# Performance work log

Measured on AMD Instinct MI355X. Metric: run time of the kernel, lower is better.

The kernel has to match this reference:

```python
import jax, jax.numpy as jnp
import numpy as np


def setup_inputs() -> dict:
    key = jax.random.key(0)
    k_z, k_w1, k_b1, k_w2, k_b2 = jax.random.split(key, 5)
    latent_dim = 16
    N = 2048
    z = jax.random.normal(k_z, (N, latent_dim), dtype=jnp.float32)
    # torch.nn.Linear default init: U(-1/sqrt(fan_in), 1/sqrt(fan_in))
    lim1 = 1.0 / np.sqrt(2 * latent_dim)
    W1 = jax.random.uniform(k_w1, (2 * latent_dim, latent_dim), minval=-lim1, maxval=lim1, dtype=jnp.float32)
    b1 = jax.random.uniform(k_b1, (latent_dim,), minval=-lim1, maxval=lim1, dtype=jnp.float32)
    lim2 = 1.0 / np.sqrt(latent_dim)
    W2 = jax.random.uniform(k_w2, (latent_dim, 1), minval=-lim2, maxval=lim2, dtype=jnp.float32)
    b2 = jax.random.uniform(k_b2, (1,), minval=-lim2, maxval=lim2, dtype=jnp.float32)
    return {"z": z, "W1": W1, "b1": b1, "W2": W2, "b2": b2}


def reference(z, W1, b1, W2, b2):
    # Pairwise concat is equivalent to splitting W1 into the halves acting on
    # z_i and z_j; we still materialize the [N, N, D] hidden like the original
    # math, but avoid the explicit [N, N, 2D] concat buffer.
    W1_i, W1_j = W1[: z.shape[1]], W1[z.shape[1] :]  # each [D, D_hidden]
    hi = z @ W1_i  # [N, Dh]
    hj = z @ W1_j  # [N, Dh]
    h = jax.nn.relu(hi[:, None, :] + hj[None, :, :] + b1)  # [N, N, Dh]
    logits = h @ W2 + b2  # [N, N, 1]
    return jax.nn.sigmoid(logits[..., 0])  # [N, N]
```

## Files before the change

kernel.cpp:

```cpp
#include <hip/hip_runtime.h>
#include <math.h>

#define D  16
#define JT 256
#define TI 32

__global__ __launch_bounds__(256) void MLPDecoder_68092411511098_kernel(
    const float* __restrict__ z, const float* __restrict__ W1,
    const float* __restrict__ b1, const float* __restrict__ W2,
    const float* __restrict__ b2, float* __restrict__ out, int N)
{
    __shared__ float sW1[2 * D * D];
    __shared__ float sZi[TI * D];
    __shared__ float sGi[TI * D];

    const int tid   = threadIdx.x;
    const int jbase = blockIdx.x * JT;
    const int ibase = blockIdx.y * TI;

    sW1[tid]       = W1[tid];
    sW1[tid + 256] = W1[tid + 256];
    if (tid < (TI * D) / 4) {
        ((float4*)sZi)[tid] = ((const float4*)(z + (size_t)ibase * D))[tid];
    }
    __syncthreads();

    float zr[D];
    {
        const float4* zrow = (const float4*)(z + (size_t)(jbase + tid) * D);
        float4 a = zrow[0], b = zrow[1], c = zrow[2], e = zrow[3];
        zr[0]=a.x;  zr[1]=a.y;  zr[2]=a.z;  zr[3]=a.w;
        zr[4]=b.x;  zr[5]=b.y;  zr[6]=b.z;  zr[7]=b.w;
        zr[8]=c.x;  zr[9]=c.y;  zr[10]=c.z; zr[11]=c.w;
        zr[12]=e.x; zr[13]=e.y; zr[14]=e.z; zr[15]=e.w;
    }
    float gj[D];
    #pragma unroll
    for (int k = 0; k < D; ++k) {
        float acc = b1[k];
        #pragma unroll
        for (int m = 0; m < D; ++m)
            acc = fmaf(zr[m], sW1[(D + m) * D + k], acc);
        gj[k] = acc;
    }

    #pragma unroll
    for (int v = tid; v < TI * D; v += 256) {
        const int ii = v >> 4, k = v & (D - 1);
        float acc = 0.0f;
        #pragma unroll
        for (int m = 0; m < D; ++m)
            acc = fmaf(sZi[ii * D + m], sW1[m * D + k], acc);
        sGi[v] = acc;
    }

    float w2r[D];
    #pragma unroll
    for (int k = 0; k < D; ++k) w2r[k] = W2[k];
    const float b2s = b2[0];
    __syncthreads();

    float* orow = out + (size_t)ibase * N + jbase + tid;
    for (int ii = 0; ii < TI; ++ii) {
        const float4* g4 = (const float4*)(sGi + ii * D);
        float4 g0 = g4[0], g1 = g4[1], g2 = g4[2], g3 = g4[3];
        float gi[D] = {g0.x,g0.y,g0.z,g0.w, g1.x,g1.y,g1.z,g1.w,
                       g2.x,g2.y,g2.z,g2.w, g3.x,g3.y,g3.z,g3.w};
        float acc = b2s;
        #pragma unroll
        for (int k = 0; k < D; ++k) {
            float t = gi[k] + gj[k];
            acc = fmaf(fmaxf(t, 0.0f), w2r[k], acc);
        }
        const float e = __expf(-acc);
        orow[(size_t)ii * N] = __builtin_amdgcn_rcpf(1.0f + e);
    }
}

extern "C" void kernel_launch(void* const* d_in, const int* in_sizes, int n_in,
                              void* d_out, int out_size, void* d_ws, size_t ws_size,
                              hipStream_t stream) {
    const float* z  = (const float*)d_in[0];
    const float* W1 = (const float*)d_in[1];
    const float* b1 = (const float*)d_in[2];
    const float* W2 = (const float*)d_in[3];
    const float* b2 = (const float*)d_in[4];
    float* out = (float*)d_out;

    const int N = in_sizes[0] / D;
    dim3 grid(N / JT, N / TI);
    MLPDecoder_68092411511098_kernel<<<grid, dim3(256), 0, stream>>>(
        z, W1, b1, W2, b2, out, N);
}
```

Measured before the change: 80.73 us.

## Precompute projections in fp16 prep kernel and use packed fdot2 inner loop

Adds a prep kernel that computes the z·W1 halves (with b1 folded into Hi) once per row and stores them as packed fp16 in the workspace. The main kernel then only loads these and does packed half add, relu and fdot2 accumulation into fp32, instead of recomputing the j-side projection in every block. TI drops from 32 to 8, giving four times as many blocks. The costs are fp16 rounding of the hidden activations, which may loosen accuracy, plus an extra kernel launch.

```diff
diff --git a/kernel.cpp b/kernel.cpp
--- a/kernel.cpp
+++ b/kernel.cpp
@@ -3,74 +3,90 @@
 
 #define D  16
 #define JT 256
-#define TI 32
+#define TI 8
+
+typedef _Float16 half2v __attribute__((ext_vector_type(2)));
+union H2U { half2v h; unsigned int u; };
+
+__global__ __launch_bounds__(256) void prep_kernel(
+    const float* __restrict__ z, const float* __restrict__ W1,
+    const float* __restrict__ b1, const float* __restrict__ W2,
+    half2v* __restrict__ Hi, half2v* __restrict__ Hj, half2v* __restrict__ w2p)
+{
+    __shared__ float sZ[16 * D];
+    __shared__ float sW[2 * D * D];
+    const int tid = threadIdx.x;
+    const int rowbase = blockIdx.x * 16;
+    if (tid < 64)       ((float4*)sZ)[tid]      = ((const float4*)(z + (size_t)rowbase * D))[tid];
+    else if (tid < 192) ((float4*)sW)[tid - 64] = ((const float4*)W1)[tid - 64];
+    __syncthreads();
+
+    const int r  = tid >> 4;
+    const int u  = tid & 15;
+    const int hf = u >> 3;
+    const int p  = u & 7;
+    const int k0 = 2 * p, k1 = k0 + 1;
+
+    float a0 = 0.f, a1 = 0.f;
+    #pragma unroll
+    for (int m = 0; m < D; ++m) {
+        const float zf = sZ[r * D + m];
+        const float* wrow = &sW[(hf * D + m) * D];
+        a0 = fmaf(zf, wrow[k0], a0);
+        a1 = fmaf(zf, wrow[k1], a1);
+    }
+    if (hf == 0) { a0 += b1[k0]; a1 += b1[k1]; }
+
+    H2U hv; hv.h.x = (_Float16)a0; hv.h.y = (_Float16)a1;
+    (hf ? Hj : Hi)[(size_t)(rowbase + r) * 8 + p] = hv.h;
+
+    if (blockIdx.x == 0 && tid < 8) {
+        H2U wv; wv.h.x = (_Float16)W2[2 * tid]; wv.h.y = (_Float16)W2[2 * tid + 1];
+        w2p[tid] = wv.h;
+    }
+}
 
 __global__ __launch_bounds__(256) void MLPDecoder_68092411511098_kernel(
-    const float* __restrict__ z, const float* __restrict__ W1,
-    const float* __restrict__ b1, const float* __restrict__ W2,
-    const float* __restrict__ b2, float* __restrict__ out, int N)
+    const half2v* __restrict__ Hi, const half2v* __restrict__ Hj,
+    const half2v* __restrict__ w2p, const float* __restrict__ b2,
+    float* __restrict__ out, int N)
 {
-    __shared__ float sW1[2 * D * D];
-    __shared__ float sZi[TI * D];
-    __shared__ float sGi[TI * D];
-
+    __shared__ half2v sHi[TI * 8];
     const int tid   = threadIdx.x;
     const int jbase = blockIdx.x * JT;
     const int ibase = blockIdx.y * TI;
 
-    sW1[tid]       = W1[tid];
-    sW1[tid + 256] = W1[tid + 256];
-    if (tid < (TI * D) / 4) {
-        ((float4*)sZi)[tid] = ((const float4*)(z + (size_t)ibase * D))[tid];
+    if (tid < TI * 8) sHi[tid] = Hi[(size_t)ibase * 8 + tid];
+
+    half2v vj[8];
+    {
+        const uint4* src = (const uint4*)(Hj + (size_t)(jbase + tid) * 8);
+        union { uint4 q; half2v h[4]; } c0, c1;
+        c0.q = src[0]; c1.q = src[1];
+        vj[0]=c0.h[0]; vj[1]=c0.h[1]; vj[2]=c0.h[2]; vj[3]=c0.h[3];
+        vj[4]=c1.h[0]; vj[5]=c1.h[1]; vj[6]=c1.h[2]; vj[7]=c1.h[3];
     }
-    __syncthreads();
-
-    float zr[D];
-    {
-        const float4* zrow = (const float4*)(z + (size_t)(jbase + tid) * D);
-        float4 a = zrow[0], b = zrow[1], c = zrow[2], e = zrow[3];
-        zr[0]=a.x;  zr[1]=a.y;  zr[2]=a.z;  zr[3]=a.w;
-        zr[4]=b.x;  zr[5]=b.y;  zr[6]=b.z;  zr[7]=b.w;
-        zr[8]=c.x;  zr[9]=c.y;  zr[10]=c.z; zr[11]=c.w;
-        zr[12]=e.x; zr[13]=e.y; zr[14]=e.z; zr[15]=e.w;
-    }
-    float gj[D];
+    half2v w2v[8];
     #pragma unroll
-    for (int k = 0; k < D; ++k) {
-        float acc = b1[k];
-        #pragma unroll
-        for (int m = 0; m < D; ++m)
-            acc = fmaf(zr[m], sW1[(D + m) * D + k], acc);
-        gj[k] = acc;
-    }
-
-    #pragma unroll
-    for (int v = tid; v < TI * D; v += 256) {
-        const int ii = v >> 4, k = v & (D - 1);
-        float acc = 0.0f;
-        #pragma unroll
-        for (int m = 0; m < D; ++m)
-            acc = fmaf(sZi[ii * D + m], sW1[m * D + k], acc);
-        sGi[v] = acc;
-    }
-
-    float w2r[D];
-    #pragma unroll
-    for (int k = 0; k < D; ++k) w2r[k] = W2[k];
+    for (int p = 0; p < 8; ++p) w2v[p] = w2p[p];
     const float b2s = b2[0];
+    const half2v zero = {(_Float16)0.f, (_Float16)0.f};
     __syncthreads();
 
     float* orow = out + (size_t)ibase * N + jbase + tid;
+    #pragma unroll 2
     for (int ii = 0; ii < TI; ++ii) {
-        const float4* g4 = (const float4*)(sGi + ii * D);
-        float4 g0 = g4[0], g1 = g4[1], g2 = g4[2], g3 = g4[3];
-        float gi[D] = {g0.x,g0.y,g0.z,g0.w, g1.x,g1.y,g1.z,g1.w,
-                       g2.x,g2.y,g2.z,g2.w, g3.x,g3.y,g3.z,g3.w};
+        const half2v* hrow = &sHi[ii * 8];
         float acc = b2s;
         #pragma unroll
-        for (int k = 0; k < D; ++k) {
-            float t = gi[k] + gj[k];
-            acc = fmaf(fmaxf(t, 0.0f), w2r[k], acc);
+        for (int p = 0; p < 8; ++p) {
+            half2v s = hrow[p] + vj[p];
+            half2v r = __builtin_elementwise_max(s, zero);
+#if __has_builtin(__builtin_amdgcn_fdot2)
+            acc = __builtin_amdgcn_fdot2(r, w2v[p], acc, false);
+#else
+            acc += (float)r.x * (float)w2v[p].x + (float)r.y * (float)w2v[p].y;
+#endif
         }
         const float e = __expf(-acc);
         orow[(size_t)ii * N] = __builtin_amdgcn_rcpf(1.0f + e);
@@ -88,7 +104,14 @@
     float* out = (float*)d_out;
 
     const int N = in_sizes[0] / D;
+
+    half2v* Hi  = (half2v*)d_ws;
+    half2v* Hj  = Hi + (size_t)N * 8;
+    half2v* w2p = Hj + (size_t)N * 8;
+
+    prep_kernel<<<dim3(N / 16), dim3(256), 0, stream>>>(z, W1, b1, W2, Hi, Hj, w2p);
+
     dim3 grid(N / JT, N / TI);
     MLPDecoder_68092411511098_kernel<<<grid, dim3(256), 0, stream>>>(
-        z, W1, b1, W2, b2, out, N);
+        Hi, Hj, w2p, b2, out, N);
 }
```

Result: faster. 73.36 us (-9.1%).

## Use packed fp16 add/relu with fdot2 for inner MLP and shrink i-tile

Applied to the files above, without the earlier changes.

The hidden activations gi and gj and the W2 weights are converted to packed half2. The inner loop uses packed fp16 add and max plus the fdot2 instruction with fp32 accumulation, which roughly halves the ALU instruction count per output. The i-tile drops from 32 to 16 rows, so the grid has more blocks, and launch bounds request 4 blocks per SM. The shared-memory prologue is reorganized so the z row load overlaps the staging of W1 and z_i, and b1 moves onto the gi side. The cost is reduced precision in the hidden layer, plus recomputing gj for twice as many blocks.

```diff
diff --git a/kernel.cpp b/kernel.cpp
--- a/kernel.cpp
+++ b/kernel.cpp
@@ -3,27 +3,22 @@
 
 #define D  16
 #define JT 256
-#define TI 32
+#define TI 16
 
-__global__ __launch_bounds__(256) void MLPDecoder_68092411511098_kernel(
+typedef _Float16 half2v __attribute__((ext_vector_type(2)));
+
+__global__ __launch_bounds__(256, 4) void MLPDecoder_68092411511098_kernel(
     const float* __restrict__ z, const float* __restrict__ W1,
     const float* __restrict__ b1, const float* __restrict__ W2,
     const float* __restrict__ b2, float* __restrict__ out, int N)
 {
-    __shared__ float sW1[2 * D * D];
-    __shared__ float sZi[TI * D];
-    __shared__ float sGi[TI * D];
+    __shared__ float  sW1[2 * D * D];
+    __shared__ float  sZi[TI * D];
+    __shared__ half2v sGi[TI * 8];
 
     const int tid   = threadIdx.x;
     const int jbase = blockIdx.x * JT;
     const int ibase = blockIdx.y * TI;
-
-    sW1[tid]       = W1[tid];
-    sW1[tid + 256] = W1[tid + 256];
-    if (tid < (TI * D) / 4) {
-        ((float4*)sZi)[tid] = ((const float4*)(z + (size_t)ibase * D))[tid];
-    }
-    __syncthreads();
 
     float zr[D];
     {
@@ -34,43 +29,66 @@
         zr[8]=c.x;  zr[9]=c.y;  zr[10]=c.z; zr[11]=c.w;
         zr[12]=e.x; zr[13]=e.y; zr[14]=e.z; zr[15]=e.w;
     }
+
+    if (tid < 128)      ((float4*)sW1)[tid]       = ((const float4*)W1)[tid];
+    else if (tid < 192) ((float4*)sZi)[tid - 128] = ((const float4*)(z + (size_t)ibase * D))[tid - 128];
+    __syncthreads();
+
     float gj[D];
     #pragma unroll
-    for (int k = 0; k < D; ++k) {
-        float acc = b1[k];
+    for (int k = 0; k < D; ++k) gj[k] = 0.0f;
+    #pragma unroll
+    for (int m = 0; m < D; ++m) {
+        const float* wrow = &sW1[(D + m) * D];
         #pragma unroll
-        for (int m = 0; m < D; ++m)
-            acc = fmaf(zr[m], sW1[(D + m) * D + k], acc);
-        gj[k] = acc;
+        for (int k = 0; k < D; ++k)
+            gj[k] = fmaf(zr[m], wrow[k], gj[k]);
+    }
+    half2v vj[8];
+    #pragma unroll
+    for (int p = 0; p < 8; ++p) {
+        vj[p].x = (_Float16)gj[2 * p];
+        vj[p].y = (_Float16)gj[2 * p + 1];
     }
 
-    #pragma unroll
-    for (int v = tid; v < TI * D; v += 256) {
-        const int ii = v >> 4, k = v & (D - 1);
-        float acc = 0.0f;
+    if (tid < TI * 8) {
+        const int r = tid >> 3, p = tid & 7;
+        const int k0 = 2 * p, k1 = k0 + 1;
+        float a0 = b1[k0], a1 = b1[k1];
         #pragma unroll
-        for (int m = 0; m < D; ++m)
-            acc = fmaf(sZi[ii * D + m], sW1[m * D + k], acc);
-        sGi[v] = acc;
+        for (int m = 0; m < D; ++m) {
+            const float zf = sZi[r * D + m];
+            a0 = fmaf(zf, sW1[m * D + k0], a0);
+            a1 = fmaf(zf, sW1[m * D + k1], a1);
+        }
+        half2v hv; hv.x = (_Float16)a0; hv.y = (_Float16)a1;
+        sGi[tid] = hv;
     }
 
-    float w2r[D];
+    half2v w2v[8];
     #pragma unroll
-    for (int k = 0; k < D; ++k) w2r[k] = W2[k];
+    for (int p = 0; p < 8; ++p) {
+        w2v[p].x = (_Float16)W2[2 * p];
+        w2v[p].y = (_Float16)W2[2 * p + 1];
+    }
     const float b2s = b2[0];
+    const half2v zero = {(_Float16)0.f, (_Float16)0.f};
     __syncthreads();
 
     float* orow = out + (size_t)ibase * N + jbase + tid;
+    #pragma unroll
     for (int ii = 0; ii < TI; ++ii) {
-        const float4* g4 = (const float4*)(sGi + ii * D);
-        float4 g0 = g4[0], g1 = g4[1], g2 = g4[2], g3 = g4[3];
-        float gi[D] = {g0.x,g0.y,g0.z,g0.w, g1.x,g1.y,g1.z,g1.w,
-                       g2.x,g2.y,g2.z,g2.w, g3.x,g3.y,g3.z,g3.w};
+        const half2v* hrow = &sGi[ii * 8];
         float acc = b2s;
         #pragma unroll
-        for (int k = 0; k < D; ++k) {
-            float t = gi[k] + gj[k];
-            acc = fmaf(fmaxf(t, 0.0f), w2r[k], acc);
+        for (int p = 0; p < 8; ++p) {
+            half2v s = hrow[p] + vj[p];
+            half2v r = __builtin_elementwise_max(s, zero);
+#if __has_builtin(__builtin_amdgcn_fdot2)
+            acc = __builtin_amdgcn_fdot2(r, w2v[p], acc, false);
+#else
+            acc += (float)r.x * (float)w2v[p].x + (float)r.y * (float)w2v[p].y;
+#endif
         }
         const float e = __expf(-acc);
         orow[(size_t)ii * N] = __builtin_amdgcn_rcpf(1.0f + e);
```

New measurement: 129.5 us. +60.4%, slower.
